# Kernel tuning notes

Hardware: AMD Instinct MI355X
Metric: run time of the kernel (lower is better)

## Reference

```python
import jax, jax.numpy as jnp
import numpy as np

T, H = 2048, 2048            # tokens, hidden_size
NQ, NKV, D = 32, 4, 128      # q heads, kv heads, head_dim
E, K, I, CAP = 64, 8, 768, 512  # experts, top_k, moe_intermediate, per-expert capacity
EPS, THETA = 1e-6, 10000.0


def setup_inputs() -> dict:
    key = jax.random.key(0)
    ks = jax.random.split(key, 10)
    n = lambda k, shp, sc: jax.random.normal(k, shp, jnp.float32) * sc
    return {
        "hidden_states": n(ks[0], (T, H), 1.0),
        "positions": jnp.arange(T, dtype=jnp.int32),
        "wqkv": n(ks[1], (H, (NQ + 2 * NKV) * D), H ** -0.5),
        "wo": n(ks[2], (NQ * D, H), (NQ * D) ** -0.5),
        "q_norm_w": jnp.ones((D,), jnp.float32),
        "k_norm_w": jnp.ones((D,), jnp.float32),
        "ln1_w": jnp.ones((H,), jnp.float32),
        "ln2_w": jnp.ones((H,), jnp.float32),
        "gate_w": n(ks[3], (H, E), H ** -0.5),
        "w_gate": n(ks[4], (E, H, I), H ** -0.5),
        "w_up": n(ks[5], (E, H, I), H ** -0.5),
        "w_down": n(ks[6], (E, I, H), I ** -0.5),
    }


def _rmsnorm(x, w):
    v = jnp.mean(jnp.square(x.astype(jnp.float32)), axis=-1, keepdims=True)
    return (x.astype(jnp.float32) * jax.lax.rsqrt(v + EPS)).astype(x.dtype) * w


def _rope(x, cos, sin):
    # x: [T, heads, D]; neox-style rotate-half over full head_dim
    x1, x2 = x[..., : D // 2], x[..., D // 2:]
    c, s = cos[:, None, :], sin[:, None, :]
    return jnp.concatenate([x1 * c - x2 * s, x2 * c + x1 * s], axis=-1)


def _forward(hidden_states, positions, wqkv, wo, q_norm_w, k_norm_w, ln1_w, ln2_w, gate_w, w_gate, w_up, w_down):
    x = hidden_states
    # ---- input RMSNorm + GQA attention with QK-norm + RoPE ----
    h = _rmsnorm(x, ln1_w)
    qkv = h @ wqkv
    q, k, v = jnp.split(qkv, [NQ * D, NQ * D + NKV * D], axis=-1)
    q = _rmsnorm(q.reshape(T, NQ, D), q_norm_w)
    k = _rmsnorm(k.reshape(T, NKV, D), k_norm_w)
    v = v.reshape(T, NKV, D)
    inv_freq = 1.0 / (THETA ** (jnp.arange(0, D, 2, dtype=jnp.float32) / D))
    ang = positions.astype(jnp.float32)[:, None] * inv_freq  # [T, D/2]
    cos, sin = jnp.cos(ang), jnp.sin(ang)
    q, k = _rope(q, cos, sin), _rope(k, cos, sin)
    rep = NQ // NKV
    kr = jnp.repeat(k, rep, axis=1)  # [T, NQ, D]
    vr = jnp.repeat(v, rep, axis=1)
    scores = jnp.einsum('qhd,khd->hqk', q, kr) * (D ** -0.5)
    causal = jnp.tril(jnp.ones((T, T), bool))
    scores = jnp.where(causal[None], scores, -1e30)
    probs = jax.nn.softmax(scores, axis=-1)
    attn = jnp.einsum('hqk,khd->qhd', probs, vr).reshape(T, NQ * D)
    x = x + attn @ wo
    # ---- post-attn RMSNorm + sparse MoE (softmax top-k routing, renormalized) ----
    h = _rmsnorm(x, ln2_w)
    logits = h @ gate_w
    gate_probs = jax.nn.softmax(logits.astype(jnp.float32), axis=-1)
    topk_w, topk_idx = jax.lax.top_k(gate_probs, K)              # [T, K]
    topk_w = topk_w / jnp.sum(topk_w, axis=-1, keepdims=True)    # norm_topk_prob
    flat_e = topk_idx.reshape(-1)                                # [T*K], row-major
    oh = jax.nn.one_hot(flat_e, E, dtype=jnp.int32)
    pos = jnp.sum(jnp.cumsum(oh, axis=0) * oh, axis=-1) - 1      # slot within expert
    x_rep = jnp.repeat(h, K, axis=0)                             # [T*K, H]
    buf = jnp.zeros((E, CAP, H), h.dtype).at[flat_e, pos].set(x_rep, mode='drop')
    g = jnp.einsum('ech,ehi->eci', buf, w_gate)
    u = jnp.einsum('ech,ehi->eci', buf, w_up)
    act = jax.nn.silu(g) * u
    out_buf = jnp.einsum('eci,eih->ech', act, w_down)
    valid = (pos < CAP).astype(h.dtype)                          # CAP >> expected load; no drops in practice
    gathered = out_buf[flat_e, jnp.clip(pos, 0, CAP - 1)]        # [T*K, H]
    w = topk_w.reshape(-1).astype(h.dtype) * valid
    moe_out = jnp.sum((gathered * w[:, None]).reshape(T, K, H), axis=1)
    return x + moe_out


def reference(hidden_states, positions, wqkv, wo, q_norm_w, k_norm_w, ln1_w, ln2_w, gate_w, w_gate, w_up, w_down):
    return _forward(hidden_states, positions, wqkv, wo, q_norm_w, k_norm_w,
                    ln1_w, ln2_w, gate_w, w_gate, w_up, w_down)
```

## Files before the change

kernel.cpp:

```cpp
#include <hip/hip_runtime.h>
#include <hip/hip_bf16.h>

#define T_    2048
#define H_    2048
#define NQ_   32
#define NKV_  4
#define D_    128
#define E_    64
#define TK_   8
#define I_    768
#define CAP_  512
#define QKVW_ 5120

typedef float  f32x4  __attribute__((ext_vector_type(4)));
typedef __bf16 bf16x8 __attribute__((ext_vector_type(8)));
typedef int    i32x4  __attribute__((ext_vector_type(4)));
#define AS1 __attribute__((address_space(1)))
#define AS3 __attribute__((address_space(3)))

static __device__ __forceinline__ unsigned f2bf_u(float f){
  unsigned u = __builtin_bit_cast(unsigned, f);
  u += 0x7fffu + ((u >> 16) & 1u);
  return u >> 16;
}
static __device__ __forceinline__ float bf2f(unsigned h){
  unsigned u = h << 16;
  return __builtin_bit_cast(float, u);
}
struct HL { int h; int l; };
static __device__ __forceinline__ HL packsplit(float a, float b){
  unsigned ah = f2bf_u(a), bh = f2bf_u(b);
  float al = a - bf2f(ah), bl = b - bf2f(bh);
  HL r;
  r.h = (int)(ah | (bh << 16));
  r.l = (int)(f2bf_u(al) | (f2bf_u(bl) << 16));
  return r;
}
static __device__ __forceinline__ f32x4 mfma16(bf16x8 a, bf16x8 b, f32x4 c){
  return __builtin_amdgcn_mfma_f32_16x16x32_bf16(a, b, c, 0, 0, 0);
}

__global__ __launch_bounds__(256) void k_rms(const float* __restrict__ in,
                                             const float* __restrict__ w,
                                             unsigned short* __restrict__ outh,
                                             unsigned short* __restrict__ outl,
                                             float* __restrict__ cpy)
{
  const int t = blockIdx.x, tid = threadIdx.x;
  const float* row = in + (long)t * H_;
  float4 a = *(const float4*)(row + tid*8);
  float4 b = *(const float4*)(row + tid*8 + 4);
  float ss = a.x*a.x + a.y*a.y + a.z*a.z + a.w*a.w
           + b.x*b.x + b.y*b.y + b.z*b.z + b.w*b.w;
  #pragma unroll
  for (int o = 32; o >= 1; o >>= 1) ss += __shfl_xor(ss, o);
  __shared__ float red[4];
  if ((tid & 63) == 0) red[tid >> 6] = ss;
  __syncthreads();
  float tot = red[0] + red[1] + red[2] + red[3];
  float rs = rsqrtf(tot * (1.0f / (float)H_) + 1e-6f);
  const float* wp = w + tid*8;
  float vv[8] = {a.x, a.y, a.z, a.w, b.x, b.y, b.z, b.w};
  i32x4 oh, ol;
  #pragma unroll
  for (int d = 0; d < 4; d++){
    float v0 = vv[2*d]   * rs * wp[2*d];
    float v1 = vv[2*d+1] * rs * wp[2*d+1];
    HL r = packsplit(v0, v1);
    oh[d] = r.h; ol[d] = r.l;
  }
  *(i32x4*)(outh + (long)t * H_ + tid*8) = oh;
  if (outl) *(i32x4*)(outl + (long)t * H_ + tid*8) = ol;
  if (cpy){
    *(float4*)(cpy + (long)t * H_ + tid*8)     = a;
    *(float4*)(cpy + (long)t * H_ + tid*8 + 4) = b;
  }
}

__global__ __launch_bounds__(64) void k_ropetab(const int* __restrict__ pos,
                                                float* __restrict__ cosb,
                                                float* __restrict__ sinb)
{
  int t = blockIdx.x, j = threadIdx.x;
  float p = (float)pos[t];
  float freq = expf(-(float)j * (2.0f / (float)D_) * 9.210340371976184f);
  float ang = p * freq;
  cosb[t*64 + j] = cosf(ang);
  sinb[t*64 + j] = sinf(ang);
}

__global__ __launch_bounds__(256) void k_qknorm(const float* __restrict__ qkv,
                                                const float* __restrict__ qw,
                                                const float* __restrict__ kw,
                                                const float* __restrict__ cosb,
                                                const float* __restrict__ sinb,
                                                unsigned short* __restrict__ qh,
                                                unsigned short* __restrict__ ql,
                                                unsigned short* __restrict__ khp,
                                                unsigned short* __restrict__ klp)
{
  int gw = blockIdx.x*4 + (threadIdx.x >> 6);
  int lane = threadIdx.x & 63;
  int t = gw / 36, hh = gw - t*36;
  const float* src; const float* w;
  unsigned short *dh, *dl;
  if (hh < NQ_){
    src = qkv + (long)t*QKVW_ + hh*D_;
    w = qw;
    dh = qh + ((long)t*NQ_ + hh)*D_;
    dl = ql + ((long)t*NQ_ + hh)*D_;
  } else {
    int kh = hh - NQ_;
    src = qkv + (long)t*QKVW_ + NQ_*D_ + kh*D_;
    w = kw;
    dh = khp + ((long)t*NKV_ + kh)*D_;
    dl = klp + ((long)t*NKV_ + kh)*D_;
  }
  float a = src[lane], b = src[lane + 64];
  float ss = a*a + b*b;
  #pragma unroll
  for (int o = 32; o >= 1; o >>= 1) ss += __shfl_xor(ss, o);
  float rs = rsqrtf(ss * (1.0f / (float)D_) + 1e-6f);
  a *= rs * w[lane];
  b *= rs * w[lane + 64];
  float c = cosb[t*64 + lane], s = sinb[t*64 + lane];
  float r0 = a*c - b*s;
  float r1 = b*c + a*s;
  unsigned h0 = f2bf_u(r0), h1 = f2bf_u(r1);
  dh[lane]      = (unsigned short)h0;
  dh[lane + 64] = (unsigned short)h1;
  dl[lane]      = (unsigned short)f2bf_u(r0 - bf2f(h0));
  dl[lane + 64] = (unsigned short)f2bf_u(r1 - bf2f(h1));
}

__global__ __launch_bounds__(256) void k_vtrans(const float* __restrict__ qkv,
                                                unsigned short* __restrict__ vth,
                                                unsigned short* __restrict__ vtl)
{
  __shared__ unsigned short tileh[64][136];
  __shared__ unsigned short tilel[64][136];
  const int t0 = blockIdx.x * 64;
  const int hv = blockIdx.y;
  const int tid = threadIdx.x;
  #pragma unroll
  for (int it = 0; it < 8; it++){
    int chunk = tid + it*256;
    int r  = chunk >> 5;
    int c4 = chunk & 31;
    float4 v = *(const float4*)(qkv + (long)(t0 + r)*QKVW_ + (NQ_+NKV_)*D_ + hv*D_ + c4*4);
    float vals[4] = {v.x, v.y, v.z, v.w};
    #pragma unroll
    for (int q = 0; q < 4; q++){
      unsigned hi = f2bf_u(vals[q]);
      tileh[r][c4*4+q] = (unsigned short)hi;
      tilel[r][c4*4+q] = (unsigned short)f2bf_u(vals[q] - bf2f(hi));
    }
  }
  __syncthreads();
  int d = tid >> 1, hf = tid & 1;
  long dbase = ((long)(hv*D_ + d))*T_ + t0 + hf*32;
  #pragma unroll
  for (int k = 0; k < 4; k++){
    i32x4 oh, ol;
    #pragma unroll
    for (int d2 = 0; d2 < 4; d2++){
      int r0 = hf*32 + k*8 + d2*2, r1 = r0 + 1;
      oh[d2] = (int)((unsigned)tileh[r0][d] | ((unsigned)tileh[r1][d] << 16));
      ol[d2] = (int)((unsigned)tilel[r0][d] | ((unsigned)tilel[r1][d] << 16));
    }
    *(i32x4*)(vth + dbase + k*8) = oh;
    *(i32x4*)(vtl + dbase + k*8) = ol;
  }
}

__global__ __launch_bounds__(256,2) void k_attn(const unsigned short* __restrict__ qbh,
                                                const unsigned short* __restrict__ qbl,
                                                const unsigned short* __restrict__ kbh,
                                                const unsigned short* __restrict__ kbl,
                                                const unsigned short* __restrict__ vth,
                                                const unsigned short* __restrict__ vtl,
                                                unsigned short* __restrict__ abh,
                                                unsigned short* __restrict__ abl)
{
  __shared__ char ldsK[2][2][16384];
  const int b   = blockIdx.x;
  const int xcd = b & 7, kk = xcd >> 1;
  const int s_  = ((b >> 3) << 1) | (xcd & 1);
  const int h   = kk*8 + (s_ >> 4);
  const int p   = s_ & 15;
  const int hk  = kk;
  const int tid = threadIdx.x;
  const int wv  = tid >> 6, lane = tid & 63;
  const int l15 = lane & 15, g16 = lane >> 4;
  const float sc = 0.08838834764831845f;

  long gb[4];
  #pragma unroll
  for (int i = 0; i < 4; i++){
    int srow = i*16 + (tid >> 4);
    int c = (tid & 15) ^ (srow & 7);
    gb[i] = ((long)srow*NKV_ + hk)*D_ + c*8;
  }

  for (int ph = 0; ph < 2; ph++){
    const int qt  = ph ? p : (31 - p);
    const int q0  = qt*64 + wv*16;
    const int ntB = qt + 1;

    bf16x8 qfh[4], qfl[4];
    {
      long qoff = ((long)(q0 + l15)*NQ_ + h)*D_ + g16*8;
      #pragma unroll
      for (int ks = 0; ks < 4; ks++){
        qfh[ks] = *(const bf16x8*)(qbh + qoff + ks*32);
        qfl[ks] = *(const bf16x8*)(qbl + qoff + ks*32);
      }
    }

    f32x4 zz = {0.f,0.f,0.f,0.f};
    f32x4 o[8];
    #pragma unroll
    for (int dn = 0; dn < 8; dn++) o[dn] = zz;
    float m_run = -1e30f, l_run = 0.f;

    __syncthreads();
    #pragma unroll
    for (int i = 0; i < 4; i++){
      __builtin_amdgcn_global_load_lds((const AS1 int*)(kbh + gb[i]),
          (AS3 int*)((AS3 char*)&ldsK[0][0][0] + i*4096 + tid*16), 16, 0, 0);
      __builtin_amdgcn_global_load_lds((const AS1 int*)(kbl + gb[i]),
          (AS3 int*)((AS3 char*)&ldsK[0][1][0] + i*4096 + tid*16), 16, 0, 0);
    }

    for (int t = 0; t < ntB; t++){
      __syncthreads();
      const int kv0 = t*64;
      if (t+1 < ntB){
        long kadd = (long)(t+1)*64*NKV_*D_;
        int nb = (t+1) & 1;
        #pragma unroll
        for (int i = 0; i < 4; i++){
          __builtin_amdgcn_global_load_lds((const AS1 int*)(kbh + gb[i] + kadd),
              (AS3 int*)((AS3 char*)&ldsK[nb][0][0] + i*4096 + tid*16), 16, 0, 0);
          __builtin_amdgcn_global_load_lds((const AS1 int*)(kbl + gb[i] + kadd),
              (AS3 int*)((AS3 char*)&ldsK[nb][1][0] + i*4096 + tid*16), 16, 0, 0);
        }
      }
      {
        const char* Kh = &ldsK[t & 1][0][0];
        const char* Kl = &ldsK[t & 1][1][0];
        f32x4 sA[4];
        #pragma unroll
        for (int sub = 0; sub < 4; sub++) sA[sub] = zz;
        __builtin_amdgcn_s_setprio(1);
        #pragma unroll
        for (int sub = 0; sub < 4; sub++){
          int row = sub*16 + l15;
          int rsw = (row & 7) << 4;
          #pragma unroll
          for (int ks = 0; ks < 4; ks++){
            bf16x8 kh = *(const bf16x8*)(Kh + row*256 + (((ks*4 + g16)*16) ^ rsw));
            bf16x8 kl = *(const bf16x8*)(Kl + row*256 + (((ks*4 + g16)*16) ^ rsw));
            sA[sub] = mfma16(kh, qfl[ks], sA[sub]);
            sA[sub] = mfma16(kl, qfh[ks], sA[sub]);
            sA[sub] = mfma16(kh, qfh[ks], sA[sub]);
          }
        }
        __builtin_amdgcn_s_setprio(0);
        {
          int qrow = q0 + l15;
          float mt = -1e30f;
          #pragma unroll
          for (int sub = 0; sub < 4; sub++)
            #pragma unroll
            for (int r = 0; r < 4; r++){
              int kva = kv0 + sub*16 + g16*4 + r;
              float v = sA[sub][r]*sc;
              if (kva > qrow) v = -1e30f;
              sA[sub][r] = v;
              mt = fmaxf(mt, v);
            }
          mt = fmaxf(mt, __shfl_xor(mt,16));
          mt = fmaxf(mt, __shfl_xor(mt,32));
          float mnew = fmaxf(m_run, mt);
          float corr = __expf(m_run - mnew);
          float ps = 0.f;
          #pragma unroll
          for (int sub = 0; sub < 4; sub++)
            #pragma unroll
            for (int r = 0; r < 4; r++){
              float e = __expf(sA[sub][r] - mnew);
              sA[sub][r] = e;
              ps += e;
            }
          ps += __shfl_xor(ps,16);
          ps += __shfl_xor(ps,32);
          l_run = l_run*corr + ps;
          m_run = mnew;
          #pragma unroll
          for (int r = 0; r < 4; r++){
            float cr = __shfl(corr, g16*4 + r);
            #pragma unroll
            for (int dn = 0; dn < 8; dn++) o[dn][r] *= cr;
          }
        }
        #pragma unroll
        for (int kst = 0; kst < 2; kst++){
          bf16x8 pah, pal;
          {
            f32x4 s0 = sA[2*kst], s1 = sA[2*kst+1];
            i32x4 pkh, pkl;
            #pragma unroll
            for (int d = 0; d < 4; d++){
              const int e0 = 2*d, e1 = 2*d+1;
              int src0 = (((2*g16 + (e0>>2)) & 3) << 4) | l15;
              int src1 = (((2*g16 + (e1>>2)) & 3) << 4) | l15;
              float a0t = __shfl(s0[e0&3], src0), a1t = __shfl(s1[e0&3], src0);
              float b0t = __shfl(s0[e1&3], src1), b1t = __shfl(s1[e1&3], src1);
              float va = (g16 >= 2) ? a1t : a0t;
              float vb = (g16 >= 2) ? b1t : b0t;
              HL r = packsplit(va, vb);
              pkh[d] = r.h; pkl[d] = r.l;
            }
            pah = __builtin_bit_cast(bf16x8, pkh);
            pal = __builtin_bit_cast(bf16x8, pkl);
          }
          __builtin_amdgcn_s_setprio(1);
          #pragma unroll
          for (int dn = 0; dn < 8; dn++){
            long voff = ((long)(hk*D_ + dn*16 + l15))*T_ + kv0 + kst*32 + g16*8;
            bf16x8 bvh = *(const bf16x8*)(vth + voff);
            bf16x8 bvl = *(const bf16x8*)(vtl + voff);
            o[dn] = mfma16(pah, bvl, o[dn]);
            o[dn] = mfma16(pal, bvh, o[dn]);
            o[dn] = mfma16(pah, bvh, o[dn]);
          }
          __builtin_amdgcn_s_setprio(0);
        }
      }
    }

    {
      float linv = 1.0f / l_run;
      #pragma unroll
      for (int r = 0; r < 4; r++){
        float lr = __shfl(linv, g16*4 + r);
        long row = q0 + g16*4 + r;
        #pragma unroll
        for (int dn = 0; dn < 8; dn++){
          float v = o[dn][r]*lr;
          unsigned hi = f2bf_u(v);
          long idx = row*(NQ_*D_) + h*D_ + dn*16 + l15;
          abh[idx] = (unsigned short)hi;
          abl[idx] = (unsigned short)f2bf_u(v - bf2f(hi));
        }
      }
    }
  }
}

struct SA {
  const unsigned short* Ah;
  const unsigned short* Al;
  const float* B;
  int lda, ldb, K, ldc;
  float* Cf;
  const float* add;
};

template<int MODE>
__global__ __launch_bounds__(256,2) void k_gs(SA ga)
{
  __shared__ unsigned short ldsAh[128*64];
  __shared__ unsigned short ldsAl[128*64];
  __shared__ unsigned short ldsBh[8*128*8];
  __shared__ unsigned short ldsBl[8*128*8];
  const int tid = threadIdx.x;
  const int lane = tid & 63;
  const int wv = tid >> 6;
  const int wm = (wv >> 1)*64, wn = (wv & 1)*64;
  const int l15 = lane & 15, g16 = lane >> 4;

  const long m0 = (long)blockIdx.y * 128;
  const long n0 = (long)blockIdx.x * 128;

  long aoff[4];
  #pragma unroll
  for (int i = 0; i < 4; i++){
    int chunk = tid + i*256;
    int m = chunk >> 3, c = chunk & 7;
    aoff[i] = (m0 + m) * (long)ga.lda + c*8;
  }
  const float* brow = ga.B + n0 + (long)((tid >> 5)*8) * ga.ldb + (tid & 31)*4;

  f32x4 zz = {0.f,0.f,0.f,0.f};
  f32x4 acc[4][4];
  #pragma unroll
  for (int i = 0; i < 4; i++)
    #pragma unroll
    for (int j = 0; j < 4; j++) acc[i][j] = zz;

  i32x4 pva[4], pvl[4];
  float4 pb[8];
  #pragma unroll
  for (int i = 0; i < 4; i++){
    pva[i] = *(const i32x4*)(ga.Ah + aoff[i]);
    pvl[i] = *(const i32x4*)(ga.Al + aoff[i]);
  }
  #pragma unroll
  for (int r = 0; r < 8; r++) pb[r] = *(const float4*)(brow + (long)r * ga.ldb);

  for (int kt = 0; kt < ga.K; kt += 64){
    __syncthreads();
    #pragma unroll
    for (int i = 0; i < 4; i++){
      int chunk = tid + i*256;
      int m = chunk >> 3, c = chunk & 7;
      int sw = (c*16) ^ ((m & 7) << 4);
      *(i32x4*)((char*)ldsAh + m*128 + sw) = pva[i];
      *(i32x4*)((char*)ldsAl + m*128 + sw) = pvl[i];
    }
    {
      i32x4 ph0, ph1, ph2, ph3, pl0, pl1, pl2, pl3;
      #pragma unroll
      for (int r = 0; r < 8; r += 2){
        float4 va = pb[r];
        float4 vb = pb[r+1];
        int d = r >> 1;
        HL rx = packsplit(va.x, vb.x); ph0[d] = rx.h; pl0[d] = rx.l;
        HL ry = packsplit(va.y, vb.y); ph1[d] = ry.h; pl1[d] = ry.l;
        HL rz = packsplit(va.z, vb.z); ph2[d] = rz.h; pl2[d] = rz.l;
        HL rw = packsplit(va.w, vb.w); ph3[d] = rw.h; pl3[d] = rw.l;
      }
      int kbb = tid >> 5, nb = (tid & 31)*4;
      long bo = ((long)kbb*128 + nb) << 4;
      char* bph = (char*)ldsBh + bo;
      char* bpl = (char*)ldsBl + bo;
      *(i32x4*)(bph)      = ph0;  *(i32x4*)(bpl)      = pl0;
      *(i32x4*)(bph + 16) = ph1;  *(i32x4*)(bpl + 16) = pl1;
      *(i32x4*)(bph + 32) = ph2;  *(i32x4*)(bpl + 32) = pl2;
      *(i32x4*)(bph + 48) = ph3;  *(i32x4*)(bpl + 48) = pl3;
    }
    __syncthreads();
    if (kt + 64 < ga.K){
      #pragma unroll
      for (int i = 0; i < 4; i++){
        pva[i] = *(const i32x4*)(ga.Ah + aoff[i] + kt + 64);
        pvl[i] = *(const i32x4*)(ga.Al + aoff[i] + kt + 64);
      }
      #pragma unroll
      for (int r = 0; r < 8; r++) pb[r] = *(const float4*)(brow + (long)(kt + 64 + r) * ga.ldb);
    }
    #pragma unroll
    for (int ks = 0; ks < 2; ks++){
      bf16x8 afh[4], afl[4], bfh[4], bfl[4];
      #pragma unroll
      for (int i = 0; i < 4; i++){
        int m = wm + i*16 + l15;
        int sw = (ks*64 + g16*16) ^ ((m & 7) << 4);
        afh[i] = *(const bf16x8*)((const char*)ldsAh + m*128 + sw);
        afl[i] = *(const bf16x8*)((const char*)ldsAl + m*128 + sw);
      }
      #pragma unroll
      for (int j = 0; j < 4; j++){
        int n = wn + j*16 + l15;
        long bo = ((long)(ks*4 + g16)*128 + n) << 4;
        bfh[j] = *(const bf16x8*)((const char*)ldsBh + bo);
        bfl[j] = *(const bf16x8*)((const char*)ldsBl + bo);
      }
      #pragma unroll
      for (int i = 0; i < 4; i++)
        #pragma unroll
        for (int j = 0; j < 4; j++){
          acc[i][j] = mfma16(afh[i], bfl[j], acc[i][j]);
          acc[i][j] = mfma16(afl[i], bfh[j], acc[i][j]);
          acc[i][j] = mfma16(afh[i], bfh[j], acc[i][j]);
        }
    }
  }

  #pragma unroll
  for (int i = 0; i < 4; i++){
    #pragma unroll
    for (int j = 0; j < 4; j++){
      #pragma unroll
      for (int r = 0; r < 4; r++){
        float v = acc[i][j][r];
        long grow = m0 + wm + i*16 + g16*4 + r;
        long gcol = n0 + wn + j*16 + l15;
        long idx = grow * ga.ldc + gcol;
        if (MODE == 0) ga.Cf[idx] = v;
        else           ga.Cf[idx] = v + ga.add[idx];
      }
    }
  }
}

struct GA {
  const unsigned short* A;
  const float* B;
  const float* B2;
  int lda, ldb, K, ldc;
  unsigned short* Cb;
  const int* rowidx;
  const float* wslot;
  const int* counts;
  float* outp;
};

template<int MODE>
__global__ __launch_bounds__(256,2) void k_gemm(GA ga)
{
  __shared__ unsigned short ldsA[128*64];
  __shared__ unsigned short ldsB[8*128*8];
  const int tid = threadIdx.x;
  const int lane = tid & 63;
  const int wv = tid >> 6;
  const int wm = (wv >> 1)*64, wn = (wv & 1)*64;
  const int l15 = lane & 15, g16 = lane >> 4;

  long m0 = (long)blockIdx.y * 128;
  long n0 = 0;
  const unsigned short* A = ga.A;
  const float* B = ga.B;
  const int* rowmap = nullptr;
  int nrows;
  int e = blockIdx.z, count = ga.counts[e], hsel = 0;
  if ((int)m0 >= count) return;
  nrows = count;

  if (MODE == 2){
    int nt = blockIdx.x;
    hsel = (nt >= 6) ? 1 : 0;
    n0 = (long)(nt - hsel*6) * 128;
    B = (hsel ? ga.B2 : ga.B) + (long)e * H_ * I_;
    rowmap = ga.rowidx + e * CAP_;
  } else {
    n0 = (long)blockIdx.x * 128;
    B = ga.B + (long)e * I_ * H_;
    A = ga.A + (long)e * CAP_ * I_;
  }

  const unsigned short* arow[4];
  #pragma unroll
  for (int i = 0; i < 4; i++){
    int chunk = tid + i*256;
    int m = chunk >> 3, c = chunk & 7;
    int s = (int)m0 + m; if (s > nrows - 1) s = nrows - 1;
    long row = (MODE == 2) ? (long)rowmap[s] : (long)s;
    arow[i] = A + row * (long)ga.lda + c*8;
  }
  const float* brow = B + n0 + (long)((tid >> 5)*8) * ga.ldb + (tid & 31)*4;

  f32x4 zz = {0.f,0.f,0.f,0.f};
  f32x4 acc[4][4];
  #pragma unroll
  for (int i = 0; i < 4; i++)
    #pragma unroll
    for (int j = 0; j < 4; j++) acc[i][j] = zz;

  i32x4 pa[4];
  float4 pb[8];
  #pragma unroll
  for (int i = 0; i < 4; i++) pa[i] = *(const i32x4*)(arow[i]);
  #pragma unroll
  for (int r = 0; r < 8; r++) pb[r] = *(const float4*)(brow + (long)r * ga.ldb);

  for (int kt = 0; kt < ga.K; kt += 64){
    __syncthreads();
    #pragma unroll
    for (int i = 0; i < 4; i++){
      int chunk = tid + i*256;
      int m = chunk >> 3, c = chunk & 7;
      *(i32x4*)((char*)ldsA + m*128 + ((c*16) ^ ((m & 7) << 4))) = pa[i];
    }
    {
      i32x4 p0, p1, p2, p3;
      #pragma unroll
      for (int r = 0; r < 8; r += 2){
        float4 va = pb[r];
        float4 vb = pb[r+1];
        int d = r >> 1;
        p0[d] = (int)(f2bf_u(va.x) | (f2bf_u(vb.x) << 16));
        p1[d] = (int)(f2bf_u(va.y) | (f2bf_u(vb.y) << 16));
        p2[d] = (int)(f2bf_u(va.z) | (f2bf_u(vb.z) << 16));
        p3[d] = (int)(f2bf_u(va.w) | (f2bf_u(vb.w) << 16));
      }
      int kbb = tid >> 5, nb = (tid & 31)*4;
      char* bp = (char*)ldsB + (((long)kbb*128 + nb) << 4);
      *(i32x4*)(bp)      = p0;
      *(i32x4*)(bp + 16) = p1;
      *(i32x4*)(bp + 32) = p2;
      *(i32x4*)(bp + 48) = p3;
    }
    __syncthreads();
    if (kt + 64 < ga.K){
      #pragma unroll
      for (int i = 0; i < 4; i++) pa[i] = *(const i32x4*)(arow[i] + kt + 64);
      #pragma unroll
      for (int r = 0; r < 8; r++) pb[r] = *(const float4*)(brow + (long)(kt + 64 + r) * ga.ldb);
    }
    #pragma unroll
    for (int ks = 0; ks < 2; ks++){
      bf16x8 af[4], bfv[4];
      #pragma unroll
      for (int i = 0; i < 4; i++){
        int m = wm + i*16 + l15;
        af[i] = *(const bf16x8*)((const char*)ldsA + m*128 + ((ks*64 + g16*16) ^ ((m & 7) << 4)));
      }
      #pragma unroll
      for (int j = 0; j < 4; j++){
        int n = wn + j*16 + l15;
        bfv[j] = *(const bf16x8*)((const char*)ldsB + (((long)(ks*4 + g16)*128 + n) << 4));
      }
      #pragma unroll
      for (int i = 0; i < 4; i++)
        #pragma unroll
        for (int j = 0; j < 4; j++)
          acc[i][j] = mfma16(af[i], bfv[j], acc[i][j]);
    }
  }

  #pragma unroll
  for (int i = 0; i < 4; i++){
    #pragma unroll
    for (int j = 0; j < 4; j++){
      #pragma unroll
      for (int r = 0; r < 4; r++){
        float v = acc[i][j][r];
        long grow = m0 + wm + i*16 + g16*4 + r;
        long gcol = n0 + wn + j*16 + l15;
        if (MODE == 2){
          if ((int)grow < count)
            ga.Cb[((long)(hsel*E_ + e)*CAP_ + grow)*I_ + gcol] = (unsigned short)f2bf_u(v);
        } else {
          if ((int)grow < count){
            float ww = ga.wslot[e*CAP_ + (int)grow];
            int tk = ga.rowidx[e*CAP_ + (int)grow];
            atomicAdd(ga.outp + (long)tk*H_ + gcol, v*ww);
          }
        }
      }
    }
  }
}

__global__ __launch_bounds__(64) void k_router(const float* __restrict__ x2,
                                               const float* __restrict__ ln2w,
                                               const float* __restrict__ gwt,
                                               int* __restrict__ tidx,
                                               float* __restrict__ twv)
{
  __shared__ float hl[H_];
  __shared__ int   ti[8];
  __shared__ float tv[8];
  const int t = blockIdx.x, lane = threadIdx.x;
  const float* row = x2 + (long)t * H_;
  float ss = 0.f;
  #pragma unroll 4
  for (int j = 0; j < 32; j++){
    float v = row[j*64 + lane];
    hl[j*64 + lane] = v;
    ss += v*v;
  }
  #pragma unroll
  for (int o = 32; o >= 1; o >>= 1) ss += __shfl_xor(ss, o);
  float rs = rsqrtf(ss * (1.0f / (float)H_) + 1e-6f);
  __syncthreads();
  #pragma unroll 4
  for (int j = 0; j < 32; j++) hl[j*64 + lane] *= rs * ln2w[j*64 + lane];
  __syncthreads();
  float acc = 0.f;
  #pragma unroll 8
  for (int k = 0; k < H_; k++) acc += hl[k] * gwt[(long)k*E_ + lane];
  float mx = acc;
  #pragma unroll
  for (int o = 32; o >= 1; o >>= 1) mx = fmaxf(mx, __shfl_xor(mx, o));
  float p = __expf(acc - mx);
  float sm = p;
  #pragma unroll
  for (int o = 32; o >= 1; o >>= 1) sm += __shfl_xor(sm, o);
  p /= sm;
  float cur = p, wsum = 0.f;
  #pragma unroll
  for (int j = 0; j < 8; j++){
    float v = cur; int ix = lane;
    #pragma unroll
    for (int o = 1; o < 64; o <<= 1){
      float ov = __shfl_xor(v, o); int oi = __shfl_xor(ix, o);
      if (ov > v || (ov == v && oi < ix)){ v = ov; ix = oi; }
    }
    if (lane == ix) cur = -1.f;
    wsum += v;
    if (lane == 0){ ti[j] = ix; tv[j] = v; }
  }
  __syncthreads();
  if (lane < 8){
    tidx[t*TK_ + lane] = ti[lane];
    twv [t*TK_ + lane] = tv[lane] / wsum;
  }
}

__global__ __launch_bounds__(64) void k_route(const int* __restrict__ tidx,
                                              const float* __restrict__ twv,
                                              int* __restrict__ rowi,
                                              float* __restrict__ wsl,
                                              int* __restrict__ cnts)
{
  const int e = blockIdx.x, lane = threadIdx.x;
  int run = 0;
  for (int s0 = 0; s0 < T_*TK_; s0 += 64){
    int s = s0 + lane;
    int idx = tidx[s];
    bool m = (idx == e);
    unsigned long long mk = __ballot(m);
    int pre = __popcll(mk & ((1ull << lane) - 1ull));
    int pos = run + pre;
    if (m && pos < CAP_){
      rowi[e*CAP_ + pos] = s >> 3;
      wsl [e*CAP_ + pos] = twv[s];
    }
    run += __popcll(mk);
  }
  if (lane == 0) cnts[e] = (run < CAP_) ? run : CAP_;
}

__global__ __launch_bounds__(256) void k_silu(unsigned short* __restrict__ gact,
                                              const unsigned short* __restrict__ uu)
{
  long i = ((long)blockIdx.x*256 + threadIdx.x)*8;
  i32x4 gv = *(const i32x4*)(gact + i);
  i32x4 uv = *(const i32x4*)(uu + i);
  i32x4 o;
  #pragma unroll
  for (int d = 0; d < 4; d++){
    unsigned gg = (unsigned)gv[d], ub = (unsigned)uv[d];
    float g0 = bf2f(gg & 0xffffu), g1 = bf2f(gg >> 16);
    float u0 = bf2f(ub & 0xffffu), u1 = bf2f(ub >> 16);
    float a0 = g0 / (1.f + __expf(-g0)) * u0;
    float a1 = g1 / (1.f + __expf(-g1)) * u1;
    o[d] = (int)(f2bf_u(a0) | (f2bf_u(a1) << 16));
  }
  *(i32x4*)(gact + i) = o;
}

extern "C" void kernel_launch(void* const* d_in, const int* in_sizes, int n_in,
                              void* d_out, int out_size, void* d_ws, size_t ws_size,
                              hipStream_t stream)
{
  (void)in_sizes; (void)n_in; (void)out_size; (void)ws_size;
  const float* x    = (const float*)d_in[0];
  const int*   pos  = (const int*)d_in[1];
  const float* wqkv = (const float*)d_in[2];
  const float* wo   = (const float*)d_in[3];
  const float* qnw  = (const float*)d_in[4];
  const float* knw  = (const float*)d_in[5];
  const float* ln1  = (const float*)d_in[6];
  const float* ln2  = (const float*)d_in[7];
  const float* gwt  = (const float*)d_in[8];
  const float* wg   = (const float*)d_in[9];
  const float* wu   = (const float*)d_in[10];
  const float* wd   = (const float*)d_in[11];
  float* out = (float*)d_out;

  char* ws = (char*)d_ws;
  size_t off = 0;
  auto alloc = [&](size_t b)->void*{ void* p = ws + off; off += (b + 255) & ~(size_t)255; return p; };

  unsigned short* hbh = (unsigned short*)alloc((size_t)T_*H_*2);
  unsigned short* hbl = (unsigned short*)alloc((size_t)T_*H_*2);
  float* qkv          = (float*)alloc((size_t)T_*QKVW_*4);
  float* cosb         = (float*)alloc((size_t)T_*64*4);
  float* sinb         = (float*)alloc((size_t)T_*64*4);
  unsigned short* qbh = (unsigned short*)alloc((size_t)T_*NQ_*D_*2);
  unsigned short* qbl = (unsigned short*)alloc((size_t)T_*NQ_*D_*2);
  unsigned short* kbh = (unsigned short*)alloc((size_t)T_*NKV_*D_*2);
  unsigned short* kbl = (unsigned short*)alloc((size_t)T_*NKV_*D_*2);
  unsigned short* vth = (unsigned short*)alloc((size_t)NKV_*D_*T_*2);
  unsigned short* vtl = (unsigned short*)alloc((size_t)NKV_*D_*T_*2);
  unsigned short* abh = (unsigned short*)alloc((size_t)T_*NQ_*D_*2);
  unsigned short* abl = (unsigned short*)alloc((size_t)T_*NQ_*D_*2);
  float* x2           = (float*)alloc((size_t)T_*H_*4);
  unsigned short* h2b = (unsigned short*)alloc((size_t)T_*H_*2);
  int* tidx           = (int*)alloc((size_t)T_*TK_*4);
  float* twv          = (float*)alloc((size_t)T_*TK_*4);
  int* rowi           = (int*)alloc((size_t)E_*CAP_*4);
  float* wsl          = (float*)alloc((size_t)E_*CAP_*4);
  int* cnts           = (int*)alloc((size_t)E_*4);
  unsigned short* gu  = (unsigned short*)alloc((size_t)2*E_*CAP_*I_*2);

  k_rms<<<T_, 256, 0, stream>>>(x, ln1, hbh, hbl, nullptr);
  k_ropetab<<<T_, 64, 0, stream>>>(pos, cosb, sinb);
  {
    SA a{}; a.Ah = hbh; a.Al = hbl; a.B = wqkv; a.lda = H_; a.ldb = QKVW_; a.K = H_; a.ldc = QKVW_; a.Cf = qkv;
    k_gs<0><<<dim3(QKVW_/128, T_/128), 256, 0, stream>>>(a);
  }
  k_qknorm<<<T_*36/4, 256, 0, stream>>>(qkv, qnw, knw, cosb, sinb, qbh, qbl, kbh, kbl);
  k_vtrans<<<dim3(T_/64, NKV_), 256, 0, stream>>>(qkv, vth, vtl);
  k_attn<<<512, 256, 0, stream>>>(qbh, qbl, kbh, kbl, vth, vtl, abh, abl);
  {
    SA a{}; a.Ah = abh; a.Al = abl; a.B = wo; a.lda = NQ_*D_; a.ldb = H_; a.K = NQ_*D_; a.ldc = H_;
    a.Cf = x2; a.add = x;
    k_gs<1><<<dim3(H_/128, T_/128), 256, 0, stream>>>(a);
  }
  k_rms<<<T_, 256, 0, stream>>>(x2, ln2, h2b, nullptr, out);
  k_router<<<T_, 64, 0, stream>>>(x2, ln2, gwt, tidx, twv);
  k_route<<<E_, 64, 0, stream>>>(tidx, twv, rowi, wsl, cnts);
  {
    GA a{}; a.A = h2b; a.B = wg; a.B2 = wu; a.lda = H_; a.ldb = I_; a.K = H_;
    a.Cb = gu; a.rowidx = rowi; a.counts = cnts;
    k_gemm<2><<<dim3(12, CAP_/128, E_), 256, 0, stream>>>(a);
  }
  k_silu<<<(E_*CAP_*I_)/(256*8), 256, 0, stream>>>(gu, gu + (size_t)E_*CAP_*I_);
  {
    GA a{}; a.A = gu; a.B = wd; a.lda = I_; a.ldb = H_; a.K = I_;
    a.counts = cnts; a.rowidx = rowi; a.wslot = wsl; a.outp = out;
    k_gemm<3><<<dim3(H_/128, CAP_/128, E_), 256, 0, stream>>>(a);
  }
}
```

Before: 1.627 ms.

## Process two 128-row M tiles per block in MoE GEMMs to reuse B tiles

Each MoE GEMM block now covers up to 256 token rows (two 128-row tiles) per expert and shares one converted bf16 B tile across both. The fp32 weight loads and bf16 conversions per block are therefore amortized over twice as many rows, halving redundant weight traffic. The cost is a doubled accumulator set (128 fp32 registers per thread), which may cut occupancy under launch_bounds(256,2), plus fewer blocks in the grid.

```diff
diff --git a/kernel.cpp b/kernel.cpp
--- a/kernel.cpp
+++ b/kernel.cpp
@@ -511,7 +511,7 @@
 template<int MODE>
 __global__ __launch_bounds__(256,2) void k_gemm(GA ga)
 {
-  __shared__ unsigned short ldsA[128*64];
+  __shared__ unsigned short ldsA[2][128*64];
   __shared__ unsigned short ldsB[8*128*8];
   const int tid = threadIdx.x;
   const int lane = tid & 63;
@@ -519,15 +519,14 @@
   const int wm = (wv >> 1)*64, wn = (wv & 1)*64;
   const int l15 = lane & 15, g16 = lane >> 4;
 
-  long m0 = (long)blockIdx.y * 128;
   long n0 = 0;
   const unsigned short* A = ga.A;
   const float* B = ga.B;
   const int* rowmap = nullptr;
-  int nrows;
   int e = blockIdx.z, count = ga.counts[e], hsel = 0;
-  if ((int)m0 >= count) return;
-  nrows = count;
+  const int mbase = (int)blockIdx.y * 256;
+  if (mbase >= count) return;
+  const int nmt = (count - mbase > 128) ? 2 : 1;
 
   if (MODE == 2){
     int nt = blockIdx.x;
@@ -541,38 +540,48 @@
     A = ga.A + (long)e * CAP_ * I_;
   }
 
-  const unsigned short* arow[4];
-  #pragma unroll
-  for (int i = 0; i < 4; i++){
-    int chunk = tid + i*256;
-    int m = chunk >> 3, c = chunk & 7;
-    int s = (int)m0 + m; if (s > nrows - 1) s = nrows - 1;
-    long row = (MODE == 2) ? (long)rowmap[s] : (long)s;
-    arow[i] = A + row * (long)ga.lda + c*8;
-  }
-  const float* brow = B + n0 + (long)((tid >> 5)*8) * ga.ldb + (tid & 31)*4;
-
-  f32x4 zz = {0.f,0.f,0.f,0.f};
-  f32x4 acc[4][4];
-  #pragma unroll
-  for (int i = 0; i < 4; i++)
-    #pragma unroll
-    for (int j = 0; j < 4; j++) acc[i][j] = zz;
-
-  i32x4 pa[4];
-  float4 pb[8];
-  #pragma unroll
-  for (int i = 0; i < 4; i++) pa[i] = *(const i32x4*)(arow[i]);
-  #pragma unroll
-  for (int r = 0; r < 8; r++) pb[r] = *(const float4*)(brow + (long)r * ga.ldb);
-
-  for (int kt = 0; kt < ga.K; kt += 64){
-    __syncthreads();
+  const unsigned short* arow[2][4];
+  #pragma unroll
+  for (int mt = 0; mt < 2; mt++)
     #pragma unroll
     for (int i = 0; i < 4; i++){
       int chunk = tid + i*256;
       int m = chunk >> 3, c = chunk & 7;
-      *(i32x4*)((char*)ldsA + m*128 + ((c*16) ^ ((m & 7) << 4))) = pa[i];
+      int s = mbase + mt*128 + m; if (s > count - 1) s = count - 1;
+      long row = (MODE == 2) ? (long)rowmap[s] : (long)s;
+      arow[mt][i] = A + row * (long)ga.lda + c*8;
+    }
+  const float* brow = B + n0 + (long)((tid >> 5)*8) * ga.ldb + (tid & 31)*4;
+
+  f32x4 zz = {0.f,0.f,0.f,0.f};
+  f32x4 acc[2][4][4];
+  #pragma unroll
+  for (int mt = 0; mt < 2; mt++)
+    #pragma unroll
+    for (int i = 0; i < 4; i++)
+      #pragma unroll
+      for (int j = 0; j < 4; j++) acc[mt][i][j] = zz;
+
+  i32x4 pa0[4], pa1[4];
+  float4 pb[8];
+  #pragma unroll
+  for (int i = 0; i < 4; i++) pa0[i] = *(const i32x4*)(arow[0][i]);
+  if (nmt == 2){
+    #pragma unroll
+    for (int i = 0; i < 4; i++) pa1[i] = *(const i32x4*)(arow[1][i]);
+  }
+  #pragma unroll
+  for (int r = 0; r < 8; r++) pb[r] = *(const float4*)(brow + (long)r * ga.ldb);
+
+  for (int kt = 0; kt < ga.K; kt += 64){
+    __syncthreads();
+    #pragma unroll
+    for (int i = 0; i < 4; i++){
+      int chunk = tid + i*256;
+      int m = chunk >> 3, c = chunk & 7;
+      int sw = m*128 + ((c*16) ^ ((m & 7) << 4));
+      *(i32x4*)((char*)&ldsA[0][0] + sw) = pa0[i];
+      if (nmt == 2) *(i32x4*)((char*)&ldsA[1][0] + sw) = pa1[i];
     }
     {
       i32x4 p0, p1, p2, p3;
@@ -596,48 +605,68 @@
     __syncthreads();
     if (kt + 64 < ga.K){
       #pragma unroll
-      for (int i = 0; i < 4; i++) pa[i] = *(const i32x4*)(arow[i] + kt + 64);
+      for (int i = 0; i < 4; i++) pa0[i] = *(const i32x4*)(arow[0][i] + kt + 64);
+      if (nmt == 2){
+        #pragma unroll
+        for (int i = 0; i < 4; i++) pa1[i] = *(const i32x4*)(arow[1][i] + kt + 64);
+      }
       #pragma unroll
       for (int r = 0; r < 8; r++) pb[r] = *(const float4*)(brow + (long)(kt + 64 + r) * ga.ldb);
     }
     #pragma unroll
     for (int ks = 0; ks < 2; ks++){
-      bf16x8 af[4], bfv[4];
-      #pragma unroll
-      for (int i = 0; i < 4; i++){
-        int m = wm + i*16 + l15;
-        af[i] = *(const bf16x8*)((const char*)ldsA + m*128 + ((ks*64 + g16*16) ^ ((m & 7) << 4)));
-      }
+      bf16x8 bfv[4];
       #pragma unroll
       for (int j = 0; j < 4; j++){
         int n = wn + j*16 + l15;
         bfv[j] = *(const bf16x8*)((const char*)ldsB + (((long)(ks*4 + g16)*128 + n) << 4));
       }
+      bf16x8 af0[4];
+      #pragma unroll
+      for (int i = 0; i < 4; i++){
+        int m = wm + i*16 + l15;
+        af0[i] = *(const bf16x8*)((const char*)&ldsA[0][0] + m*128 + ((ks*64 + g16*16) ^ ((m & 7) << 4)));
+      }
       #pragma unroll
       for (int i = 0; i < 4; i++)
         #pragma unroll
         for (int j = 0; j < 4; j++)
-          acc[i][j] = mfma16(af[i], bfv[j], acc[i][j]);
-    }
-  }
-
-  #pragma unroll
-  for (int i = 0; i < 4; i++){
-    #pragma unroll
-    for (int j = 0; j < 4; j++){
-      #pragma unroll
-      for (int r = 0; r < 4; r++){
-        float v = acc[i][j][r];
-        long grow = m0 + wm + i*16 + g16*4 + r;
-        long gcol = n0 + wn + j*16 + l15;
-        if (MODE == 2){
-          if ((int)grow < count)
-            ga.Cb[((long)(hsel*E_ + e)*CAP_ + grow)*I_ + gcol] = (unsigned short)f2bf_u(v);
-        } else {
-          if ((int)grow < count){
-            float ww = ga.wslot[e*CAP_ + (int)grow];
-            int tk = ga.rowidx[e*CAP_ + (int)grow];
-            atomicAdd(ga.outp + (long)tk*H_ + gcol, v*ww);
+          acc[0][i][j] = mfma16(af0[i], bfv[j], acc[0][i][j]);
+      if (nmt == 2){
+        bf16x8 af1[4];
+        #pragma unroll
+        for (int i = 0; i < 4; i++){
+          int m = wm + i*16 + l15;
+          af1[i] = *(const bf16x8*)((const char*)&ldsA[1][0] + m*128 + ((ks*64 + g16*16) ^ ((m & 7) << 4)));
+        }
+        #pragma unroll
+        for (int i = 0; i < 4; i++)
+          #pragma unroll
+          for (int j = 0; j < 4; j++)
+            acc[1][i][j] = mfma16(af1[i], bfv[j], acc[1][i][j]);
+      }
+    }
+  }
+
+  for (int mt = 0; mt < nmt; mt++){
+    #pragma unroll
+    for (int i = 0; i < 4; i++){
+      #pragma unroll
+      for (int j = 0; j < 4; j++){
+        #pragma unroll
+        for (int r = 0; r < 4; r++){
+          float v = acc[mt][i][j][r];
+          int grow = mbase + mt*128 + wm + i*16 + g16*4 + r;
+          long gcol = n0 + wn + j*16 + l15;
+          if (MODE == 2){
+            if (grow < count)
+              ga.Cb[((long)(hsel*E_ + e)*CAP_ + grow)*I_ + gcol] = (unsigned short)f2bf_u(v);
+          } else {
+            if (grow < count){
+              float ww = ga.wslot[e*CAP_ + grow];
+              int tk = ga.rowidx[e*CAP_ + grow];
+              atomicAdd(ga.outp + (long)tk*H_ + gcol, v*ww);
+            }
           }
         }
       }
@@ -809,12 +838,12 @@
   {
     GA a{}; a.A = h2b; a.B = wg; a.B2 = wu; a.lda = H_; a.ldb = I_; a.K = H_;
     a.Cb = gu; a.rowidx = rowi; a.counts = cnts;
-    k_gemm<2><<<dim3(12, CAP_/128, E_), 256, 0, stream>>>(a);
+    k_gemm<2><<<dim3(12, 2, E_), 256, 0, stream>>>(a);
   }
   k_silu<<<(E_*CAP_*I_)/(256*8), 256, 0, stream>>>(gu, gu + (size_t)E_*CAP_*I_);
   {
     GA a{}; a.A = gu; a.B = wd; a.lda = I_; a.ldb = H_; a.K = I_;
     a.counts = cnts; a.rowidx = rowi; a.wslot = wsl; a.outp = out;
-    k_gemm<3><<<dim3(H_/128, CAP_/128, E_), 256, 0, stream>>>(a);
-  }
-}
+    k_gemm<3><<<dim3(16, 2, E_), 256, 0, stream>>>(a);
+  }
+}
```

Result: slower. 2.938 ms (+80.6%).
